# Kernel optimization log

Measured on AMD Instinct MI355X. Metric: run time of the kernel, lower is better.

Reference implementation:

```python
import jax, jax.numpy as jnp
import numpy as np

L = 4
N_STEPS = 8
H_OSC = 0.1   # self.h passed to oscillator layers
H_WAVE = 0.1  # hard-coded in WaveLayer(h=0.1)


def _forward(x, edge_index, root_idx, key_emb, val_emb, linear_w, linear_b,
             osc_a, osc_Bw, osc_Bb, final_w):
    n = x.shape[0]
    d = key_emb.shape[1]
    row, col = edge_index[0], edge_index[1]
    # in-degree of aggregation targets (col), recomputed once (constant over steps)
    deg = jax.ops.segment_sum(jnp.ones(row.shape[0], dtype=key_emb.dtype), col,
                              num_segments=n)

    # initial node encoding
    X = key_emb[x[:, 0]] + val_emb[x[:, 1]]                 # [n, d]
    X = jax.nn.relu(jnp.einsum('nd,od->no', X, linear_w) + linear_b)
    Y = jnp.zeros_like(X)
    Z = jnp.zeros((L, n, d), dtype=X.dtype)
    U = jnp.zeros((L, n, d), dtype=X.dtype)

    def osc(z, z_prev, u, j):
        # u_new = u + h*relu(a*z + B z_prev + b); z_new = z + h*u_new
        u_new = u + H_OSC * jax.nn.relu(
            osc_a[j] * z + jnp.einsum('nd,od->no', z_prev, osc_Bw[j]) + osc_Bb[j])
        z_new = z + H_OSC * u_new
        return z_new, u_new

    def step(carry, _):
        X, Y, Z, U = carry
        # WaveLayer (normalized_lap=False, self_loops=False):
        # vel_update = deg*x - scatter_add(x[row] -> col)  (graph Laplacian)
        agg = jax.ops.segment_sum(-X[row], col, num_segments=n)  # [n, d]
        vel_update = deg[:, None] * X + agg
        Y = Y - H_WAVE * vel_update
        X = X + H_WAVE * Y
        # oscillator stack, same update order as the torch loop
        z0, u0 = osc(Z[0], X, U[0], 0)
        Z = Z.at[0].set(z0)
        U = U.at[0].set(u0)
        for j in range(L - 1, 0, -1):
            zj, uj = osc(Z[j], Z[j - 1], U[j], j)
            Z = Z.at[j].set(zj)
            U = U.at[j].set(uj)
        return (X, Y, Z, U), None

    (X, Y, Z, U), _ = jax.lax.scan(step, (X, Y, Z, U), None, length=N_STEPS)
    z_roots = Z[L - 1][root_idx]                            # [R, d]
    return jnp.einsum('rd,od->ro', z_roots, final_w)        # [R, output_dim+1]


def setup_inputs() -> dict:
    n, input_dim, d, out_dim, R = 50000, 32, 64, 10, 1024
    rng = np.random.default_rng(0)
    # undirected edge list (to_undirected): symmetrize + dedupe
    e0 = 400000
    src = rng.integers(0, n, e0)
    dst = rng.integers(0, n, e0)
    e = np.stack([np.concatenate([src, dst]), np.concatenate([dst, src])])
    e = np.unique(e, axis=1)
    key = jax.random.key(0)
    ks = jax.random.split(key, 9)
    s = 1.0 / np.sqrt(d)
    return {
        'x': jax.random.randint(ks[0], (n, 2), 0, input_dim + 1, dtype=jnp.int32),
        'edge_index': jnp.asarray(e, dtype=jnp.int32),
        'root_idx': jax.random.randint(ks[1], (R,), 0, n, dtype=jnp.int32),
        'key_emb': jax.random.normal(ks[2], (input_dim + 1, d), jnp.float32),
        'val_emb': jax.random.normal(ks[3], (input_dim + 1, d), jnp.float32),
        'linear_w': jax.random.normal(ks[4], (d, d), jnp.float32) * s,
        'linear_b': jnp.zeros((d,), jnp.float32),
        'osc_a': jax.random.normal(ks[5], (L, d), jnp.float32) * 0.1,
        'osc_Bw': jax.random.normal(ks[6], (L, d, d), jnp.float32) * s,
        'osc_Bb': jnp.zeros((L, d), jnp.float32),
        'final_w': jax.random.normal(ks[7], (out_dim + 1, d), jnp.float32) * s,
    }


def reference(x, edge_index, root_idx, key_emb, val_emb, linear_w, linear_b,
              osc_a, osc_Bw, osc_Bb, final_w):
    return _forward(x, edge_index, root_idx, key_emb, val_emb, linear_w, linear_b,
                    osc_a, osc_Bw, osc_Bb, final_w)
```

## Files before the change

kernel.cpp:

```cpp
#include <hip/hip_runtime.h>

#define H 0.1f

typedef float float4v __attribute__((ext_vector_type(4)));

__device__ __forceinline__ float bcast_lane(float v, int l) {
    return __int_as_float(__builtin_amdgcn_readlane(__float_as_int(v), l));
}

__global__ void __launch_bounds__(256) prep1_kernel(
    const float* __restrict__ key_emb, const float* __restrict__ val_emb,
    const float* __restrict__ lw, const float* __restrict__ lb,
    float* __restrict__ Wk, float* __restrict__ Wv, int K,
    const int* __restrict__ erow, int* __restrict__ ptr, int n, int E,
    const int* __restrict__ roots, int* __restrict__ mask, int R,
    int TBLK, int BBLK)
{
    const int bid = blockIdx.x;
    if (bid < TBLK) {
        const int wv = bid * 4 + ((int)threadIdx.x >> 6);
        const int lane = threadIdx.x & 63;
        if (wv < 2 * K) {
            const int which = wv >= K;
            const int k = which ? wv - K : wv;
            float4v wreg[16];
            const float* wp = lw + (size_t)lane * 64;
#pragma unroll
            for (int q = 0; q < 16; ++q) wreg[q] = *(const float4v*)(wp + 4 * q);
            const float* emb = which ? val_emb : key_emb;
            float ev = emb[k * 64 + lane];
            float acc = which ? 0.f : lb[lane];
#pragma unroll
            for (int q = 0; q < 16; ++q)
#pragma unroll
                for (int j = 0; j < 4; ++j)
                    acc = fmaf(bcast_lane(ev, 4 * q + j), wreg[q][j], acc);
            (which ? Wv : Wk)[k * 64 + lane] = acc;
        }
    } else if (bid < TBLK + BBLK) {
        int e = (bid - TBLK) * 256 + threadIdx.x;
        if (e < E) {
            int b = erow[e];
            int a = (e == 0) ? -1 : erow[e - 1];
            for (int v = a + 1; v <= b; ++v) ptr[v] = e;
            if (e == E - 1)
                for (int v = b + 1; v <= n; ++v) ptr[v] = E;
        }
    } else {
        int i = (bid - TBLK - BBLK) * 256 + threadIdx.x;
        if (i < R) mask[roots[i]] = 1;
    }
}

__global__ void __launch_bounds__(256) prep2_kernel(
    const int* __restrict__ xnode, const float* __restrict__ Wk,
    const float* __restrict__ Wv, float* __restrict__ X0, int n,
    const int* __restrict__ erow, const int* __restrict__ ecol,
    const int* __restrict__ mask, int* __restrict__ mask2, int E, int IBLK)
{
    const int bid = blockIdx.x;
    if (bid < IBLK) {
        const int lane = threadIdx.x & 63;
        const int v = (bid * 256 + (int)threadIdx.x) >> 6;
        if (v < n) {
            unsigned k0 = (unsigned)__builtin_amdgcn_readfirstlane(xnode[2 * v + 0]);
            unsigned k1 = (unsigned)__builtin_amdgcn_readfirstlane(xnode[2 * v + 1]);
            float p = Wk[(k0 << 6) + lane] + Wv[(k1 << 6) + lane];
            X0[((unsigned)v << 6) + lane] = p > 0.f ? p : 0.f;
        }
    } else {
        int e = (bid - IBLK) * 256 + threadIdx.x;
        if (e < E && mask[erow[e]]) mask2[ecol[e]] = 1;
    }
}

template <bool MASKED>
__global__ void __launch_bounds__(256) wave_step4(
    const float* __restrict__ Xin, const float* __restrict__ Xm1,
    float* __restrict__ Xout, const int* __restrict__ ptr,
    const int* __restrict__ csr, int n,
    const int* __restrict__ mask, const int* __restrict__ mask2)
{
    const int lane = threadIdx.x & 63;
    const int v = (blockIdx.x * blockDim.x + threadIdx.x) >> 6;
    if (v >= n) return;
    if (MASKED) {
        if (!(__builtin_amdgcn_readfirstlane(mask[v]) |
              __builtin_amdgcn_readfirstlane(mask2[v]))) return;
    }
    const int g = lane >> 4;
    const int c = lane & 15;
    int b = __builtin_amdgcn_readfirstlane(ptr[v]);
    int e = __builtin_amdgcn_readfirstlane(ptr[v + 1]);

    const float4v* Xq = (const float4v*)Xin + c;
    float4v a0 = {0.f, 0.f, 0.f, 0.f}, a1 = {0.f, 0.f, 0.f, 0.f};
    int k = b + g;
    for (; k + 4 < e; k += 8) {
        unsigned i0 = (unsigned)csr[k] << 4;
        unsigned i1 = (unsigned)csr[k + 4] << 4;
        a0 += Xq[i0];
        a1 += Xq[i1];
    }
    if (k < e) a0 += Xq[(unsigned)csr[k] << 4];
    float4v s4 = a0 + a1;
#pragma unroll
    for (int j = 0; j < 4; ++j) {
        float t = s4[j];
        t += __shfl_xor(t, 16);
        t += __shfl_xor(t, 32);
        s4[j] = t;
    }

    const unsigned q = ((unsigned)v << 4) + c;
    float4v x4 = ((const float4v*)Xin)[q];
    float4v xm14 = ((const float4v*)Xm1)[q];
    const float deg = (float)(e - b);
    float4v xn;
#pragma unroll
    for (int j = 0; j < 4; ++j) {
        float lap = fmaf(deg, x4[j], -s4[j]);
        xn[j] = fmaf(-(H * H), lap, (x4[j] + x4[j]) - xm14[j]);
    }
    if (g == 0) ((float4v*)Xout)[q] = xn;
}

__device__ __forceinline__ float wave_update(
    const float* __restrict__ Xin, float x, float xm1, int lane, int b, int e,
    const int* __restrict__ csr)
{
    const float* Xl = Xin + lane;
    float s0 = 0.f, s1 = 0.f, s2 = 0.f, s3 = 0.f;
    float s4 = 0.f, s5 = 0.f, s6 = 0.f, s7 = 0.f;
    int k = b;
    for (; k + 8 <= e; k += 8) {
        unsigned n0 = (unsigned)csr[k + 0], n1 = (unsigned)csr[k + 1];
        unsigned n2 = (unsigned)csr[k + 2], n3 = (unsigned)csr[k + 3];
        unsigned n4 = (unsigned)csr[k + 4], n5 = (unsigned)csr[k + 5];
        unsigned n6 = (unsigned)csr[k + 6], n7 = (unsigned)csr[k + 7];
        s0 += Xl[n0 << 6];
        s1 += Xl[n1 << 6];
        s2 += Xl[n2 << 6];
        s3 += Xl[n3 << 6];
        s4 += Xl[n4 << 6];
        s5 += Xl[n5 << 6];
        s6 += Xl[n6 << 6];
        s7 += Xl[n7 << 6];
    }
    if (k + 4 <= e) {
        unsigned n0 = (unsigned)csr[k + 0], n1 = (unsigned)csr[k + 1];
        unsigned n2 = (unsigned)csr[k + 2], n3 = (unsigned)csr[k + 3];
        s0 += Xl[n0 << 6];
        s1 += Xl[n1 << 6];
        s2 += Xl[n2 << 6];
        s3 += Xl[n3 << 6];
        k += 4;
    }
    for (; k < e; ++k) s0 += Xl[(unsigned)csr[k] << 6];
    float s = ((s0 + s1) + (s2 + s3)) + ((s4 + s5) + (s6 + s7));
    float lap = fmaf((float)(e - b), x, -s);
    return fmaf(-(H * H), lap, (x + x) - xm1);
}

__global__ void __launch_bounds__(64) root_osc_final(
    const float* __restrict__ Xall, const int* __restrict__ roots,
    const float* __restrict__ osc_a, const float* __restrict__ Bw,
    const float* __restrict__ Bb, const float* __restrict__ fw,
    const int* __restrict__ ptr, const int* __restrict__ csr,
    float* __restrict__ out, int n, int R, int nout, size_t nd)
{
    const int lane = threadIdx.x;
    const int r = blockIdx.x;
    if (r >= R) return;
    const int v = __builtin_amdgcn_readfirstlane(roots[r]);

    const float* P7 = Xall + 7 * nd;
    const float* P6 = Xall + 6 * nd;
    const unsigned base = ((unsigned)v << 6) + lane;
    int b = __builtin_amdgcn_readfirstlane(ptr[v]);
    int e = __builtin_amdgcn_readfirstlane(ptr[v + 1]);
    float x8 = wave_update(P7, P7[base], P6[base], lane, b, e, csr);

    float hin[9], hout[9];

    {
        float4v wreg[16];
        const float* wp = Bw + (size_t)lane * 64;
#pragma unroll
        for (int q = 0; q < 16; ++q) wreg[q] = *(const float4v*)(wp + 4 * q);
        const float aj = osc_a[lane];
        const float bj = Bb[lane];
        float z = 0.f, u = 0.f;
#pragma unroll
        for (int s = 1; s <= 8; ++s) {
            float zp = (s < 8) ? Xall[(size_t)s * nd + base] : x8;
            float acc = fmaf(aj, z, bj);
#pragma unroll
            for (int q = 0; q < 16; ++q)
#pragma unroll
                for (int j = 0; j < 4; ++j)
                    acc = fmaf(bcast_lane(zp, 4 * q + j), wreg[q][j], acc);
            float t = acc > 0.f ? acc : 0.f;
            u += H * t;
            z += H * u;
            hout[s] = z;
        }
    }

    auto pass = [&](int j, int prev_step) {
        float4v wreg[16];
        const float* wp = Bw + (size_t)j * 4096 + (size_t)lane * 64;
#pragma unroll
        for (int q = 0; q < 16; ++q) wreg[q] = *(const float4v*)(wp + 4 * q);
        const float aj = osc_a[j * 64 + lane];
        const float bj = Bb[j * 64 + lane];
        float z = 0.f, u = 0.f;
#pragma unroll
        for (int s = 1; s <= 8; ++s) {
            float zp = prev_step ? hin[s - 1] : hin[s];
            float acc = fmaf(aj, z, bj);
#pragma unroll
            for (int q = 0; q < 16; ++q)
#pragma unroll
                for (int jj = 0; jj < 4; ++jj)
                    acc = fmaf(bcast_lane(zp, 4 * q + jj), wreg[q][jj], acc);
            float t = acc > 0.f ? acc : 0.f;
            u += H * t;
            z += H * u;
            hout[s] = z;
        }
    };

    hin[0] = 0.f;
#pragma unroll
    for (int i = 1; i <= 8; ++i) hin[i] = hout[i];
    pass(1, 0);
    hin[0] = 0.f;
#pragma unroll
    for (int i = 1; i <= 8; ++i) hin[i] = hout[i];
    pass(2, 1);
    hin[0] = 0.f;
#pragma unroll
    for (int i = 1; i <= 8; ++i) hin[i] = hout[i];
    pass(3, 1);

    float z3 = hout[8];
    for (int o = 0; o < nout; ++o) {
        float p = z3 * fw[o * 64 + lane];
#pragma unroll
        for (int off = 32; off > 0; off >>= 1)
            p += __shfl_xor(p, off);
        if (lane == 0) out[r * nout + o] = p;
    }
}

extern "C" void kernel_launch(void* const* d_in, const int* in_sizes, int n_in,
                              void* d_out, int out_size, void* d_ws, size_t ws_size,
                              hipStream_t stream)
{
    const int*   xnode   = (const int*)d_in[0];
    const int*   edge    = (const int*)d_in[1];
    const int*   roots   = (const int*)d_in[2];
    const float* key_emb = (const float*)d_in[3];
    const float* val_emb = (const float*)d_in[4];
    const float* lw      = (const float*)d_in[5];
    const float* lb      = (const float*)d_in[6];
    const float* osc_a   = (const float*)d_in[7];
    const float* Bw      = (const float*)d_in[8];
    const float* Bb      = (const float*)d_in[9];
    const float* fw      = (const float*)d_in[10];

    const int n = in_sizes[0] / 2;
    const int E = in_sizes[1] / 2;
    const int R = in_sizes[2];
    const int K = in_sizes[3] / 64;
    const int nout = out_size / R;
    const int* erow = edge;
    const int* ecol = edge + E;

    const size_t nd = (size_t)n * 64;
    float* Xall  = (float*)d_ws;
    float* Wk    = Xall + 8 * nd;
    float* Wv    = Wk + (size_t)K * 64;
    int*   ptr   = (int*)(Wv + (size_t)K * 64);
    int*   mask  = ptr + n + 1;
    int*   mask2 = mask + n;

    hipMemsetAsync(mask, 0, (size_t)(2 * n) * sizeof(int), stream);

    const int TBLK = (2 * K + 3) / 4;
    const int BBLK = (E + 255) / 256;
    const int RBLK = (R + 255) / 256;
    prep1_kernel<<<TBLK + BBLK + RBLK, 256, 0, stream>>>(
        key_emb, val_emb, lw, lb, Wk, Wv, K, erow, ptr, n, E,
        roots, mask, R, TBLK, BBLK);

    const int IBLK = (n * 64 + 255) / 256;
    const int MBLK = (E + 255) / 256;
    prep2_kernel<<<IBLK + MBLK, 256, 0, stream>>>(
        xnode, Wk, Wv, Xall, n, erow, ecol, mask, mask2, E, IBLK);

    const int nblocks = (n + 3) / 4;
    for (int s = 1; s <= 6; ++s) {
        const float* xin = Xall + (size_t)(s - 1) * nd;
        const float* xm1 = (s == 1) ? xin : Xall + (size_t)(s - 2) * nd;
        wave_step4<false><<<nblocks, 256, 0, stream>>>(
            xin, xm1, Xall + (size_t)s * nd, ptr, ecol, n, nullptr, nullptr);
    }
    wave_step4<true><<<nblocks, 256, 0, stream>>>(
        Xall + 6 * nd, Xall + 5 * nd, Xall + 7 * nd, ptr, ecol, n, mask, mask2);

    root_osc_final<<<R, 64, 0, stream>>>(
        Xall, roots, osc_a, Bw, Bb, fw, ptr, ecol,
        (float*)d_out, n, R, nout, nd);
}
```

Measured before the change: 256.1 us.

## Process two nodes per wavefront with interleaved scalar-per-lane neighbor gathers

Replaces the wave-step kernel, which split one node's neighbor list across four 16-lane groups loading float4, with a kernel where each 64-lane wavefront handles two nodes. Each lane gathers one float per neighbor, and the two neighbor lists are walked together with four accumulators each. This removes the cross-group shuffle reduction and the idle lanes on the store, and keeps more independent loads in flight per wave. The cost is narrower per-lane loads, half as many wavefronts, and load imbalance when the two nodes have different degrees. The previous-step buffer is now read with nontemporal loads.

Result: slower. 269.6 us (+5.3%).

```diff
diff --git a/kernel.cpp b/kernel.cpp
--- a/kernel.cpp
+++ b/kernel.cpp
@@ -75,54 +75,87 @@
 }
 
 template <bool MASKED>
-__global__ void __launch_bounds__(256) wave_step4(
+__global__ void __launch_bounds__(256) wave_step2(
     const float* __restrict__ Xin, const float* __restrict__ Xm1,
     float* __restrict__ Xout, const int* __restrict__ ptr,
     const int* __restrict__ csr, int n,
     const int* __restrict__ mask, const int* __restrict__ mask2)
 {
     const int lane = threadIdx.x & 63;
-    const int v = (blockIdx.x * blockDim.x + threadIdx.x) >> 6;
-    if (v >= n) return;
+    const int w = (int)((blockIdx.x * blockDim.x + threadIdx.x) >> 6);
+    const int v0 = w * 2;
+    if (v0 >= n) return;
+    const int v1 = v0 + 1;
+    bool aA = true, aB = (v1 < n);
     if (MASKED) {
-        if (!(__builtin_amdgcn_readfirstlane(mask[v]) |
-              __builtin_amdgcn_readfirstlane(mask2[v]))) return;
-    }
-    const int g = lane >> 4;
-    const int c = lane & 15;
-    int b = __builtin_amdgcn_readfirstlane(ptr[v]);
-    int e = __builtin_amdgcn_readfirstlane(ptr[v + 1]);
-
-    const float4v* Xq = (const float4v*)Xin + c;
-    float4v a0 = {0.f, 0.f, 0.f, 0.f}, a1 = {0.f, 0.f, 0.f, 0.f};
-    int k = b + g;
-    for (; k + 4 < e; k += 8) {
-        unsigned i0 = (unsigned)csr[k] << 4;
-        unsigned i1 = (unsigned)csr[k + 4] << 4;
-        a0 += Xq[i0];
-        a1 += Xq[i1];
-    }
-    if (k < e) a0 += Xq[(unsigned)csr[k] << 4];
-    float4v s4 = a0 + a1;
-#pragma unroll
-    for (int j = 0; j < 4; ++j) {
-        float t = s4[j];
-        t += __shfl_xor(t, 16);
-        t += __shfl_xor(t, 32);
-        s4[j] = t;
-    }
-
-    const unsigned q = ((unsigned)v << 4) + c;
-    float4v x4 = ((const float4v*)Xin)[q];
-    float4v xm14 = ((const float4v*)Xm1)[q];
-    const float deg = (float)(e - b);
-    float4v xn;
-#pragma unroll
-    for (int j = 0; j < 4; ++j) {
-        float lap = fmaf(deg, x4[j], -s4[j]);
-        xn[j] = fmaf(-(H * H), lap, (x4[j] + x4[j]) - xm14[j]);
-    }
-    if (g == 0) ((float4v*)Xout)[q] = xn;
+        aA = (__builtin_amdgcn_readfirstlane(mask[v0]) |
+              __builtin_amdgcn_readfirstlane(mask2[v0])) != 0;
+        if (aB)
+            aB = (__builtin_amdgcn_readfirstlane(mask[v1]) |
+                  __builtin_amdgcn_readfirstlane(mask2[v1])) != 0;
+        if (!aA && !aB) return;
+    }
+    int b0 = __builtin_amdgcn_readfirstlane(ptr[v0]);
+    int m  = __builtin_amdgcn_readfirstlane(ptr[v1]);
+    int e1 = aB ? __builtin_amdgcn_readfirstlane(ptr[v0 + 2]) : m;
+
+    const float* Xl = Xin + lane;
+    float sA0 = 0.f, sA1 = 0.f, sA2 = 0.f, sA3 = 0.f;
+    float sB0 = 0.f, sB1 = 0.f, sB2 = 0.f, sB3 = 0.f;
+    int kA = aA ? b0 : m;
+    int kB = m;
+
+    while (kA + 4 <= m && kB + 4 <= e1) {
+        unsigned a0 = (unsigned)csr[kA + 0], a1 = (unsigned)csr[kA + 1];
+        unsigned a2 = (unsigned)csr[kA + 2], a3 = (unsigned)csr[kA + 3];
+        unsigned c0 = (unsigned)csr[kB + 0], c1 = (unsigned)csr[kB + 1];
+        unsigned c2 = (unsigned)csr[kB + 2], c3 = (unsigned)csr[kB + 3];
+        sA0 += Xl[a0 << 6];
+        sA1 += Xl[a1 << 6];
+        sA2 += Xl[a2 << 6];
+        sA3 += Xl[a3 << 6];
+        sB0 += Xl[c0 << 6];
+        sB1 += Xl[c1 << 6];
+        sB2 += Xl[c2 << 6];
+        sB3 += Xl[c3 << 6];
+        kA += 4;
+        kB += 4;
+    }
+    for (; kA + 4 <= m; kA += 4) {
+        unsigned a0 = (unsigned)csr[kA + 0], a1 = (unsigned)csr[kA + 1];
+        unsigned a2 = (unsigned)csr[kA + 2], a3 = (unsigned)csr[kA + 3];
+        sA0 += Xl[a0 << 6];
+        sA1 += Xl[a1 << 6];
+        sA2 += Xl[a2 << 6];
+        sA3 += Xl[a3 << 6];
+    }
+    for (; kA < m; ++kA) sA0 += Xl[(unsigned)csr[kA] << 6];
+    for (; kB + 4 <= e1; kB += 4) {
+        unsigned c0 = (unsigned)csr[kB + 0], c1 = (unsigned)csr[kB + 1];
+        unsigned c2 = (unsigned)csr[kB + 2], c3 = (unsigned)csr[kB + 3];
+        sB0 += Xl[c0 << 6];
+        sB1 += Xl[c1 << 6];
+        sB2 += Xl[c2 << 6];
+        sB3 += Xl[c3 << 6];
+    }
+    for (; kB < e1; ++kB) sB0 += Xl[(unsigned)csr[kB] << 6];
+
+    if (aA) {
+        const unsigned base0 = ((unsigned)v0 << 6) + lane;
+        float x = Xin[base0];
+        float xm1 = __builtin_nontemporal_load(&Xm1[base0]);
+        float s = (sA0 + sA1) + (sA2 + sA3);
+        float lap = fmaf((float)(m - b0), x, -s);
+        Xout[base0] = fmaf(-(H * H), lap, (x + x) - xm1);
+    }
+    if (aB) {
+        const unsigned base1 = ((unsigned)v1 << 6) + lane;
+        float x = Xin[base1];
+        float xm1 = __builtin_nontemporal_load(&Xm1[base1]);
+        float s = (sB0 + sB1) + (sB2 + sB3);
+        float lap = fmaf((float)(e1 - m), x, -s);
+        Xout[base1] = fmaf(-(H * H), lap, (x + x) - xm1);
+    }
 }
 
 __device__ __forceinline__ float wave_update(
@@ -300,14 +333,15 @@
     prep2_kernel<<<IBLK + MBLK, 256, 0, stream>>>(
         xnode, Wk, Wv, Xall, n, erow, ecol, mask, mask2, E, IBLK);
 
-    const int nblocks = (n + 3) / 4;
+    const int nwaves  = (n + 1) / 2;
+    const int nblocks = (nwaves + 3) / 4;
     for (int s = 1; s <= 6; ++s) {
         const float* xin = Xall + (size_t)(s - 1) * nd;
         const float* xm1 = (s == 1) ? xin : Xall + (size_t)(s - 2) * nd;
-        wave_step4<false><<<nblocks, 256, 0, stream>>>(
+        wave_step2<false><<<nblocks, 256, 0, stream>>>(
             xin, xm1, Xall + (size_t)s * nd, ptr, ecol, n, nullptr, nullptr);
     }
-    wave_step4<true><<<nblocks, 256, 0, stream>>>(
+    wave_step2<true><<<nblocks, 256, 0, stream>>>(
         Xall + 6 * nd, Xall + 5 * nd, Xall + 7 * nd, ptr, ecol, n, mask, mask2);
 
     root_osc_final<<<R, 64, 0, stream>>>(
```
